# Performance work log

Hardware: AMD Instinct MI355X
Metric: run time of the kernel (lower is better)

## Reference

```python
import jax, jax.numpy as jnp
import numpy as np

N = 100000
E = 1600000
E_OUT = 400000
IN_DIM = 16
HID = 64
OUT_DIM = 2
L = 6
BN_EPS = 1e-5


def setup_inputs() -> dict:
    key = jax.random.key(0)
    ks = jax.random.split(key, 12)
    x = jax.random.normal(ks[0], (N, IN_DIM), dtype=jnp.float32)
    edge_index = jax.random.randint(ks[1], (2, E), 0, N, dtype=jnp.int64)
    edge_index_out = jax.random.randint(ks[2], (2, E_OUT), 0, N, dtype=jnp.int64)
    s_emb = 1.0 / np.sqrt(IN_DIM)
    s_hid = 1.0 / np.sqrt(HID)
    W_emb = jax.random.uniform(ks[3], (IN_DIM, HID), jnp.float32, -s_emb, s_emb)
    b_emb = jax.random.uniform(ks[4], (HID,), jnp.float32, -s_emb, s_emb)
    conv_W = jax.random.uniform(ks[5], (L, HID, HID), jnp.float32, -s_hid, s_hid)
    conv_b = jnp.zeros((L, HID), jnp.float32)
    bn_gamma = jnp.ones((L, HID), jnp.float32)
    bn_beta = jnp.zeros((L, HID), jnp.float32)
    s_fc = 1.0 / np.sqrt(2 * HID)
    fc_W = jax.random.uniform(ks[6], (2 * HID, OUT_DIM), jnp.float32, -s_fc, s_fc)
    fc_b = jax.random.uniform(ks[7], (OUT_DIM,), jnp.float32, -s_fc, s_fc)
    return dict(x=x, edge_index=edge_index, edge_index_out=edge_index_out,
                W_emb=W_emb, b_emb=b_emb, conv_W=conv_W, conv_b=conv_b,
                bn_gamma=bn_gamma, bn_beta=bn_beta, fc_W=fc_W, fc_b=fc_b)


def gcn_conv(h, W, b, src, dst, norm):
    # PyG GCNConv: h' = scatter_add(norm * (hW)[src] -> dst) + b
    hw = h @ W                                   # [N, HID]
    msgs = hw[src] * norm[:, None]               # [E+N, HID] gather
    agg = jax.ops.segment_sum(msgs, dst, num_segments=N)
    return agg + b


def batchnorm_train(h, gamma, beta):
    mean = jnp.mean(h, axis=0)
    var = jnp.mean(jnp.square(h - mean), axis=0)  # biased var (BN training)
    return (h - mean) * jax.lax.rsqrt(var + BN_EPS) * gamma + beta


def reference(x, edge_index, edge_index_out, W_emb, b_emb, conv_W, conv_b,
              bn_gamma, bn_beta, fc_W, fc_b):
    # add self-loops + symmetric normalization (computed once, shared by layers)
    loop = jnp.arange(N, dtype=edge_index.dtype)
    src = jnp.concatenate([edge_index[0], loop])
    dst = jnp.concatenate([edge_index[1], loop])
    deg = jax.ops.segment_sum(jnp.ones_like(dst, dtype=jnp.float32), dst, num_segments=N)
    dinv = jnp.where(deg > 0, jax.lax.rsqrt(jnp.maximum(deg, 1.0)), 0.0)
    norm = dinv[src] * dinv[dst]

    x_embed = x @ W_emb + b_emb                  # node embedding [N, HID]
    for i in range(L):
        h = gcn_conv(x_embed, conv_W[i], conv_b[i], src, dst, norm)
        h = jax.nn.relu(batchnorm_train(h, bn_gamma[i], bn_beta[i]))
        x_embed = x_embed + h                    # residual

    e_src, e_dst = edge_index_out[0], edge_index_out[1]
    edge_repr = jnp.concatenate([x_embed[e_src], x_embed[e_dst]], axis=-1)  # [E_out, 2*HID]
    return edge_repr @ fc_W + fc_b
```

## Files before the change

### kernel.cpp

```cpp
#include <hip/hip_runtime.h>

#define NN 100000
#define NE 1600000
#define NEO 400000
#define HID 64
#define NL 6
#define BN_EPS 1e-5f

#define SPMM_BLOCKS 6250
#define SCAN_BS 512
#define SCAN_NB 196
#define GRP_ROWS 12500
#define BUILD_BPG 784

#define OFF_ECOL 0
#define OFF_XE   NE
#define OFF_AGG  (OFF_XE + NN * 32)
#define OFF_HWB  (OFF_AGG + NN * 32)

#define OD_DINV   0
#define OD_ROWPTR 100352
#define OD_CC     200704
#define OD_BSUM   300704
#define OD_SS     300960
#define OD_SUMS   301088

typedef __attribute__((ext_vector_type(8))) short bf16x8;
typedef __attribute__((ext_vector_type(4))) float f32x4;

static __device__ __forceinline__ unsigned short f2bf(float f) {
    unsigned u = __float_as_uint(f);
    unsigned r = (u + 0x7FFF + ((u >> 16) & 1)) >> 16;
    return (unsigned short)r;
}
static __device__ __forceinline__ float bflo(unsigned u) {
    return __uint_as_float(u << 16);
}
static __device__ __forceinline__ float bfhi(unsigned u) {
    return __uint_as_float(u & 0xFFFF0000u);
}

__global__ void k_hist(const int* __restrict__ dst, int* __restrict__ cnt) {
    int e = blockIdx.x * blockDim.x + threadIdx.x;
    if (e < NE) atomicAdd(&cnt[dst[e]], 1);
}

__global__ void k_scanA(const int* __restrict__ cnt, int* __restrict__ rowptr,
                        int* __restrict__ bsum, float* __restrict__ dinv) {
    __shared__ int sh[SCAN_BS];
    int t = threadIdx.x;
    int i = blockIdx.x * SCAN_BS + t;
    int v = (i < NN) ? cnt[i] : 0;
    sh[t] = v;
    __syncthreads();
    for (int off = 1; off < SCAN_BS; off <<= 1) {
        int a = (t >= off) ? sh[t - off] : 0;
        __syncthreads();
        sh[t] += a;
        __syncthreads();
    }
    if (i < NN) {
        rowptr[i] = sh[t] - v;
        dinv[i] = rsqrtf((float)(v + 1));
    }
    if (t == SCAN_BS - 1) bsum[blockIdx.x] = sh[t];
}

__global__ void k_scanB(int* __restrict__ bsum) {
    __shared__ int sh[256];
    int t = threadIdx.x;
    int v = (t < SCAN_NB) ? bsum[t] : 0;
    sh[t] = v;
    __syncthreads();
    for (int off = 1; off < 256; off <<= 1) {
        int a = (t >= off) ? sh[t - off] : 0;
        __syncthreads();
        sh[t] += a;
        __syncthreads();
    }
    if (t < SCAN_NB) bsum[t] = (t == 0) ? 0 : sh[t - 1];
}

__global__ void k_scanC(int* __restrict__ rowptr, const int* __restrict__ bsum,
                        int* __restrict__ cursor) {
    int i = blockIdx.x * SCAN_BS + threadIdx.x;
    if (i < NN) {
        int rp = rowptr[i] + bsum[blockIdx.x];
        rowptr[i] = rp;
        cursor[i] = rp;
    }
    if (i == 0) rowptr[NN] = NE;
}

__global__ void k_build(const int* __restrict__ src, const int* __restrict__ dst,
                        int* __restrict__ cursor, int* __restrict__ ecol) {
    int g = blockIdx.x & 7;
    int b = blockIdx.x >> 3;
    int lo = g * GRP_ROWS, hi = lo + GRP_ROWS;
    for (int e = b * blockDim.x + threadIdx.x; e < NE; e += BUILD_BPG * blockDim.x) {
        int d = dst[e];
        if (d >= lo && d < hi) {
            int pos = atomicAdd(&cursor[d], 1);
            ecol[pos] = src[e];
        }
    }
}

__global__ void k_embed(const float* __restrict__ x, const float* __restrict__ W,
                        const float* __restrict__ b, unsigned short* __restrict__ xe16) {
    __shared__ float Ws[16 * 64];
    __shared__ float bs[64];
    int t = threadIdx.x;
    for (int i = t; i < 16 * 64; i += 256) Ws[i] = W[i];
    if (t < 64) bs[t] = b[t];
    __syncthreads();
    int c = t & 63, r = t >> 6;
    int n0 = blockIdx.x * 64;
    for (int n = n0 + r; n < n0 + 64 && n < NN; n += 4) {
        const float* xr = x + n * 16;
        float acc = bs[c];
#pragma unroll
        for (int k = 0; k < 16; k++) acc = fmaf(xr[k], Ws[k * 64 + c], acc);
        xe16[(size_t)n * 64 + c] = f2bf(acc);
    }
}

__global__ void k_hw(unsigned short* __restrict__ xe16,
                     const float* __restrict__ W, const float* __restrict__ dinv,
                     const unsigned short* __restrict__ agg16,
                     const float* __restrict__ gamma, const float* __restrict__ beta,
                     const double* __restrict__ sumsPrev, double* __restrict__ sumsCur,
                     unsigned short* __restrict__ hwb, int apply) {
    __shared__ unsigned short Wt[64 * 72];
    __shared__ unsigned short Xb[64 * 72];
    __shared__ float sss[128];
    int t = threadIdx.x;
    int n0 = blockIdx.x * 64;
    if (blockIdx.x == 0) {
        for (int i = t; i < 2048; i += 256) sumsCur[i] = 0.0;
    }
    if (apply && t < 64) {
        double s = 0.0, q = 0.0;
#pragma unroll
        for (int k = 0; k < 16; k++) {
            s += sumsPrev[k * 128 + t];
            q += sumsPrev[k * 128 + 64 + t];
        }
        double mean = s / (double)NN;
        double var = q / (double)NN - mean * mean;
        float sc = gamma[t] * rsqrtf((float)var + BN_EPS);
        sss[t] = sc;
        sss[64 + t] = beta[t] - (float)mean * sc;
    }

    {
        int c = t & 63, r = t >> 6;
#pragma unroll
        for (int jj = 0; jj < 4; jj++) {
            float w0 = W[(r * 16 + jj * 4 + 0) * 64 + c];
            float w1 = W[(r * 16 + jj * 4 + 1) * 64 + c];
            float w2 = W[(r * 16 + jj * 4 + 2) * 64 + c];
            float w3 = W[(r * 16 + jj * 4 + 3) * 64 + c];
            uint2 pk;
            pk.x = ((unsigned)f2bf(w1) << 16) | f2bf(w0);
            pk.y = ((unsigned)f2bf(w3) << 16) | f2bf(w2);
            *(uint2*)&Wt[c * 72 + r * 16 + jj * 4] = pk;
        }
    }
    __syncthreads();

    {
        int n = t >> 2, kq = t & 3;
        int node = n0 + n;
        unsigned xs[8] = {0, 0, 0, 0, 0, 0, 0, 0};
        if (node < NN) {
            const uint4* xr = (const uint4*)(xe16 + (size_t)node * 64 + kq * 16);
            uint4 x0 = xr[0], x1 = xr[1];
            xs[0] = x0.x; xs[1] = x0.y; xs[2] = x0.z; xs[3] = x0.w;
            xs[4] = x1.x; xs[5] = x1.y; xs[6] = x1.z; xs[7] = x1.w;
            if (apply) {
                const uint4* ar = (const uint4*)(agg16 + (size_t)node * 64 + kq * 16);
                uint4 a0 = ar[0], a1 = ar[1];
                unsigned as[8] = {a0.x, a0.y, a0.z, a0.w, a1.x, a1.y, a1.z, a1.w};
                int c = kq * 16;
#pragma unroll
                for (int i = 0; i < 8; i++) {
                    float v0 = bflo(xs[i]) +
                               fmaxf(fmaf(bflo(as[i]), sss[c + 2 * i], sss[64 + c + 2 * i]), 0.f);
                    float v1 = bfhi(xs[i]) +
                               fmaxf(fmaf(bfhi(as[i]), sss[c + 2 * i + 1], sss[64 + c + 2 * i + 1]), 0.f);
                    xs[i] = ((unsigned)f2bf(v1) << 16) | f2bf(v0);
                }
                uint4* xw = (uint4*)(xe16 + (size_t)node * 64 + kq * 16);
                xw[0] = make_uint4(xs[0], xs[1], xs[2], xs[3]);
                xw[1] = make_uint4(xs[4], xs[5], xs[6], xs[7]);
            }
        }
        *(uint4*)&Xb[n * 72 + kq * 16] = make_uint4(xs[0], xs[1], xs[2], xs[3]);
        *(uint4*)&Xb[n * 72 + kq * 16 + 8] = make_uint4(xs[4], xs[5], xs[6], xs[7]);
    }
    __syncthreads();

    int lane = t & 63, w = t >> 6;
    int m = lane & 15, quad = lane >> 4;
    f32x4 acc[4];
#pragma unroll
    for (int tc = 0; tc < 4; tc++) acc[tc] = (f32x4){0.f, 0.f, 0.f, 0.f};
#pragma unroll
    for (int s = 0; s < 2; s++) {
        bf16x8 bfr = *(const bf16x8*)&Xb[(w * 16 + m) * 72 + s * 32 + quad * 8];
#pragma unroll
        for (int tc = 0; tc < 4; tc++) {
            bf16x8 afr = *(const bf16x8*)&Wt[(tc * 16 + m) * 72 + s * 32 + quad * 8];
            acc[tc] = __builtin_amdgcn_mfma_f32_16x16x32_bf16(afr, bfr, acc[tc], 0, 0, 0);
        }
    }
    int node = n0 + w * 16 + m;
    if (node < NN) {
        float di = dinv[node];
#pragma unroll
        for (int tc = 0; tc < 4; tc++) {
            int c0 = tc * 16 + quad * 4;
            uint2 pk;
            pk.x = ((unsigned)f2bf(acc[tc][1] * di) << 16) | f2bf(acc[tc][0] * di);
            pk.y = ((unsigned)f2bf(acc[tc][3] * di) << 16) | f2bf(acc[tc][2] * di);
            *(uint2*)(hwb + (size_t)node * 64 + c0) = pk;
        }
    }
}

__global__ void k_spmm(const int* __restrict__ rowptr, const int* __restrict__ ecol,
                       const unsigned short* __restrict__ hwb, const float* __restrict__ dinv,
                       unsigned short* __restrict__ agg16, double* __restrict__ sums) {
    int t = threadIdx.x;
    int w = t >> 6, l = t & 63;
    int r = l >> 4;
    int sub = (l >> 3) & 1;
    int q = l & 7;
    const uint4* hw4 = (const uint4*)hwb;
    float ls[8], lq[8];
#pragma unroll
    for (int j = 0; j < 8; j++) { ls[j] = 0.f; lq[j] = 0.f; }
    for (int row0 = blockIdx.x * 16 + w * 4; row0 < NN; row0 += SPMM_BLOCKS * 16) {
        int row = row0 + r;
        bool valid = row < NN;
        int p0 = 0, p1 = 0;
        float a[8];
#pragma unroll
        for (int j = 0; j < 8; j++) a[j] = 0.f;
        if (valid) {
            p0 = rowptr[row];
            p1 = rowptr[row + 1];
            if (sub == 0) {
                uint4 sv = hw4[(size_t)row * 8 + q];
                a[0] = bflo(sv.x); a[1] = bfhi(sv.x); a[2] = bflo(sv.y); a[3] = bfhi(sv.y);
                a[4] = bflo(sv.z); a[5] = bfhi(sv.z); a[6] = bflo(sv.w); a[7] = bfhi(sv.w);
            }
        }
        int p = p0 + sub;
        for (; p + 2 < p1; p += 4) {
            int s0 = ecol[p], s1 = ecol[p + 2];
            uint4 u0 = hw4[(size_t)s0 * 8 + q];
            uint4 u1 = hw4[(size_t)s1 * 8 + q];
            a[0] += bflo(u0.x); a[1] += bfhi(u0.x); a[2] += bflo(u0.y); a[3] += bfhi(u0.y);
            a[4] += bflo(u0.z); a[5] += bfhi(u0.z); a[6] += bflo(u0.w); a[7] += bfhi(u0.w);
            a[0] += bflo(u1.x); a[1] += bfhi(u1.x); a[2] += bflo(u1.y); a[3] += bfhi(u1.y);
            a[4] += bflo(u1.z); a[5] += bfhi(u1.z); a[6] += bflo(u1.w); a[7] += bfhi(u1.w);
        }
        if (p < p1) {
            int s0 = ecol[p];
            uint4 u0 = hw4[(size_t)s0 * 8 + q];
            a[0] += bflo(u0.x); a[1] += bfhi(u0.x); a[2] += bflo(u0.y); a[3] += bfhi(u0.y);
            a[4] += bflo(u0.z); a[5] += bfhi(u0.z); a[6] += bflo(u0.w); a[7] += bfhi(u0.w);
        }
#pragma unroll
        for (int j = 0; j < 8; j++) a[j] += __shfl_xor(a[j], 8, 64);
        if (valid && sub == 0) {
            float di = dinv[row];
            unsigned pk[4];
#pragma unroll
            for (int j = 0; j < 4; j++) {
                float v0 = a[2 * j] * di, v1 = a[2 * j + 1] * di;
                pk[j] = ((unsigned)f2bf(v1) << 16) | f2bf(v0);
            }
            *(uint4*)(agg16 + (size_t)row * 64 + 8 * q) = make_uint4(pk[0], pk[1], pk[2], pk[3]);
#pragma unroll
            for (int j = 0; j < 4; j++) {
                float v0 = bflo(pk[j]), v1 = bfhi(pk[j]);
                ls[2 * j] += v0; ls[2 * j + 1] += v1;
                lq[2 * j] = fmaf(v0, v0, lq[2 * j]);
                lq[2 * j + 1] = fmaf(v1, v1, lq[2 * j + 1]);
            }
        }
    }
#pragma unroll
    for (int j = 0; j < 8; j++) {
        ls[j] += __shfl_xor(ls[j], 16, 64); ls[j] += __shfl_xor(ls[j], 32, 64);
        lq[j] += __shfl_xor(lq[j], 16, 64); lq[j] += __shfl_xor(lq[j], 32, 64);
    }
    __shared__ float Ss[4][64], Sq[4][64];
    if (l < 8) {
#pragma unroll
        for (int j = 0; j < 8; j++) {
            Ss[w][8 * l + j] = ls[j];
            Sq[w][8 * l + j] = lq[j];
        }
    }
    __syncthreads();
    if (t < 64) {
        float a = Ss[0][t] + Ss[1][t] + Ss[2][t] + Ss[3][t];
        float b = Sq[0][t] + Sq[1][t] + Sq[2][t] + Sq[3][t];
        double* sh = sums + (blockIdx.x & 15) * 128;
        atomicAdd(&sh[t], (double)a);
        atomicAdd(&sh[64 + t], (double)b);
    }
}

__global__ void k_finalize(const double* __restrict__ sums, const float* __restrict__ gamma,
                           const float* __restrict__ beta, float* __restrict__ ss) {
    int c = threadIdx.x;
    double s = 0.0, q = 0.0;
#pragma unroll
    for (int k = 0; k < 16; k++) { s += sums[k * 128 + c]; q += sums[k * 128 + 64 + c]; }
    double mean = s / (double)NN;
    double var = q / (double)NN - mean * mean;
    float sc = gamma[c] * rsqrtf((float)var + BN_EPS);
    ss[c] = sc;
    ss[64 + c] = beta[c] - (float)mean * sc;
}

__global__ void k_apply(const unsigned short* __restrict__ agg16, const float* __restrict__ ss,
                        unsigned short* __restrict__ xe16) {
    int i = blockIdx.x * blockDim.x + threadIdx.x;
    if (i < NN * 8) {
        int c0 = (i & 7) * 8;
        uint4 av = *(const uint4*)(agg16 + (size_t)i * 8);
        uint4 xv = *(const uint4*)(xe16 + (size_t)i * 8);
        unsigned as[4] = {av.x, av.y, av.z, av.w};
        unsigned xs[4] = {xv.x, xv.y, xv.z, xv.w};
#pragma unroll
        for (int j = 0; j < 4; j++) {
            int c = c0 + 2 * j;
            float v0 = bflo(xs[j]) + fmaxf(fmaf(bflo(as[j]), ss[c], ss[64 + c]), 0.f);
            float v1 = bfhi(xs[j]) + fmaxf(fmaf(bfhi(as[j]), ss[c + 1], ss[64 + c + 1]), 0.f);
            xs[j] = ((unsigned)f2bf(v1) << 16) | f2bf(v0);
        }
        *(uint4*)(xe16 + (size_t)i * 8) = make_uint4(xs[0], xs[1], xs[2], xs[3]);
    }
}

__global__ void k_out(const int* __restrict__ esrc, const int* __restrict__ edst,
                      const unsigned short* __restrict__ xe16, const float* __restrict__ fcW,
                      const float* __restrict__ fcb, float* __restrict__ out) {
    __shared__ float Ws[256];
    __shared__ float bs[2];
    int t = threadIdx.x;
    for (int i = t; i < 256; i += 256) Ws[i] = fcW[i];
    if (t < 2) bs[t] = fcb[t];
    __syncthreads();
    int e = blockIdx.x * blockDim.x + t;
    if (e < NEO) {
        int s = esrc[e], d = edst[e];
        const uint4* rs = (const uint4*)(xe16 + (size_t)s * 64);
        const uint4* rd = (const uint4*)(xe16 + (size_t)d * 64);
        float a0 = bs[0], a1 = bs[1];
#pragma unroll
        for (int i = 0; i < 8; i++) {
            uint4 v = rs[i];
            int c = i * 8;
            a0 += bflo(v.x) * Ws[(c + 0) * 2] + bfhi(v.x) * Ws[(c + 1) * 2] +
                  bflo(v.y) * Ws[(c + 2) * 2] + bfhi(v.y) * Ws[(c + 3) * 2] +
                  bflo(v.z) * Ws[(c + 4) * 2] + bfhi(v.z) * Ws[(c + 5) * 2] +
                  bflo(v.w) * Ws[(c + 6) * 2] + bfhi(v.w) * Ws[(c + 7) * 2];
            a1 += bflo(v.x) * Ws[(c + 0) * 2 + 1] + bfhi(v.x) * Ws[(c + 1) * 2 + 1] +
                  bflo(v.y) * Ws[(c + 2) * 2 + 1] + bfhi(v.y) * Ws[(c + 3) * 2 + 1] +
                  bflo(v.z) * Ws[(c + 4) * 2 + 1] + bfhi(v.z) * Ws[(c + 5) * 2 + 1] +
                  bflo(v.w) * Ws[(c + 6) * 2 + 1] + bfhi(v.w) * Ws[(c + 7) * 2 + 1];
        }
#pragma unroll
        for (int i = 0; i < 8; i++) {
            uint4 v = rd[i];
            int c = 64 + i * 8;
            a0 += bflo(v.x) * Ws[(c + 0) * 2] + bfhi(v.x) * Ws[(c + 1) * 2] +
                  bflo(v.y) * Ws[(c + 2) * 2] + bfhi(v.y) * Ws[(c + 3) * 2] +
                  bflo(v.z) * Ws[(c + 4) * 2] + bfhi(v.z) * Ws[(c + 5) * 2] +
                  bflo(v.w) * Ws[(c + 6) * 2] + bfhi(v.w) * Ws[(c + 7) * 2];
            a1 += bflo(v.x) * Ws[(c + 0) * 2 + 1] + bfhi(v.x) * Ws[(c + 1) * 2 + 1] +
                  bflo(v.y) * Ws[(c + 2) * 2 + 1] + bfhi(v.y) * Ws[(c + 3) * 2 + 1] +
                  bflo(v.z) * Ws[(c + 4) * 2 + 1] + bfhi(v.z) * Ws[(c + 5) * 2 + 1] +
                  bflo(v.w) * Ws[(c + 6) * 2 + 1] + bfhi(v.w) * Ws[(c + 7) * 2 + 1];
        }
        out[e * 2] = a0;
        out[e * 2 + 1] = a1;
    }
}

extern "C" void kernel_launch(void* const* d_in, const int* in_sizes, int n_in,
                              void* d_out, int out_size, void* d_ws, size_t ws_size,
                              hipStream_t stream) {
    const float* x      = (const float*)d_in[0];
    const int*   ei     = (const int*)d_in[1];
    const int*   eio    = (const int*)d_in[2];
    const float* W_emb  = (const float*)d_in[3];
    const float* b_emb  = (const float*)d_in[4];
    const float* conv_W = (const float*)d_in[5];
    const float* bn_g   = (const float*)d_in[7];
    const float* bn_b   = (const float*)d_in[8];
    const float* fc_W   = (const float*)d_in[9];
    const float* fc_b   = (const float*)d_in[10];
    float* out = (float*)d_out;

    float* ws   = (float*)d_ws;
    int*   ecol = (int*)(ws + OFF_ECOL);
    unsigned short* xe16  = (unsigned short*)(ws + OFF_XE);
    unsigned short* agg16 = (unsigned short*)(ws + OFF_AGG);
    unsigned short* hwb   = (unsigned short*)(ws + OFF_HWB);

    float* od     = (float*)d_out;
    float* dinv   = od + OD_DINV;
    int*   rowptr = (int*)(od + OD_ROWPTR);
    int*   cc     = (int*)(od + OD_CC);
    int*   bsum   = (int*)(od + OD_BSUM);
    float* ss     = od + OD_SS;
    double* sums  = (double*)(od + OD_SUMS);

    const int* src  = ei;
    const int* dst  = ei + NE;
    const int* esrc = eio;
    const int* edst = eio + NEO;

    (void)hipMemsetAsync(cc, 0, NN * sizeof(int), stream);
    k_hist<<<(NE + 255) / 256, 256, 0, stream>>>(dst, cc);
    k_scanA<<<SCAN_NB, SCAN_BS, 0, stream>>>(cc, rowptr, bsum, dinv);
    k_scanB<<<1, 256, 0, stream>>>(bsum);
    k_scanC<<<SCAN_NB, SCAN_BS, 0, stream>>>(rowptr, bsum, cc);
    k_build<<<8 * BUILD_BPG, 256, 0, stream>>>(src, dst, cc, ecol);

    k_embed<<<(NN + 63) / 64, 256, 0, stream>>>(x, W_emb, b_emb, xe16);

    for (int l = 0; l < NL; l++) {
        double* sumsPrev = sums + ((l + 1) & 1) * 2048;
        double* sumsCur  = sums + (l & 1) * 2048;
        k_hw<<<(NN + 63) / 64, 256, 0, stream>>>(xe16, conv_W + l * 64 * 64, dinv, agg16,
                                                 bn_g + (l ? (l - 1) * 64 : 0),
                                                 bn_b + (l ? (l - 1) * 64 : 0),
                                                 sumsPrev, sumsCur, hwb, l > 0 ? 1 : 0);
        k_spmm<<<SPMM_BLOCKS, 256, 0, stream>>>(rowptr, ecol, hwb, dinv, agg16, sumsCur);
    }
    k_finalize<<<1, 64, 0, stream>>>(sums + ((NL - 1) & 1) * 2048,
                                     bn_g + (NL - 1) * 64, bn_b + (NL - 1) * 64, ss);
    k_apply<<<(NN * 8 + 255) / 256, 256, 0, stream>>>(agg16, ss, xe16);

    k_out<<<(NEO + 255) / 256, 256, 0, stream>>>(esrc, edst, xe16, fc_W, fc_b, out);
}
```

Baseline: 576.5 us.

## Pre-bin edges by destination group before CSR build

```diff
diff --git a/kernel.cpp b/kernel.cpp
--- a/kernel.cpp
+++ b/kernel.cpp
@@ -11,7 +11,11 @@
 #define SCAN_BS 512
 #define SCAN_NB 196
 #define GRP_ROWS 12500
-#define BUILD_BPG 784
+
+#define BIN_CHUNK 2048
+#define BIN_BLOCKS ((NE + BIN_CHUNK - 1) / BIN_CHUNK)
+#define BIN_CAP 210000
+#define B2_BPG 98
 
 #define OFF_ECOL 0
 #define OFF_XE   NE
@@ -24,6 +28,7 @@
 #define OD_BSUM   300704
 #define OD_SS     300960
 #define OD_SUMS   301088
+#define OD_GCUR   309280
 
 typedef __attribute__((ext_vector_type(8))) short bf16x8;
 typedef __attribute__((ext_vector_type(4))) float f32x4;
@@ -40,9 +45,37 @@
     return __uint_as_float(u & 0xFFFF0000u);
 }
 
-__global__ void k_hist(const int* __restrict__ dst, int* __restrict__ cnt) {
-    int e = blockIdx.x * blockDim.x + threadIdx.x;
-    if (e < NE) atomicAdd(&cnt[dst[e]], 1);
+__global__ void k_bin(const int* __restrict__ src, const int* __restrict__ dst,
+                      int* __restrict__ cnt, int* __restrict__ gcur,
+                      int* __restrict__ bsrc, int* __restrict__ bdst) {
+    __shared__ int cnt8[8], base8[8], off8[8];
+    int t = threadIdx.x;
+    if (t < 8) { cnt8[t] = 0; off8[t] = 0; }
+    __syncthreads();
+    int cb = blockIdx.x * BIN_CHUNK;
+    int s[8], d[8], g[8];
+#pragma unroll
+    for (int j = 0; j < 8; j++) {
+        int e = cb + t + j * 256;
+        s[j] = (e < NE) ? src[e] : -1;
+        d[j] = (e < NE) ? dst[e] : -1;
+        if (d[j] >= 0) {
+            g[j] = (unsigned)d[j] / GRP_ROWS;
+            atomicAdd(&cnt8[g[j]], 1);
+            atomicAdd(&cnt[d[j]], 1);
+        }
+    }
+    __syncthreads();
+    if (t < 8) base8[t] = t * BIN_CAP + atomicAdd(&gcur[t], cnt8[t]);
+    __syncthreads();
+#pragma unroll
+    for (int j = 0; j < 8; j++) {
+        if (d[j] >= 0) {
+            int pos = base8[g[j]] + atomicAdd(&off8[g[j]], 1);
+            bsrc[pos] = s[j];
+            bdst[pos] = d[j];
+        }
+    }
 }
 
 __global__ void k_scanA(const int* __restrict__ cnt, int* __restrict__ rowptr,
@@ -92,17 +125,18 @@
     if (i == 0) rowptr[NN] = NE;
 }
 
-__global__ void k_build(const int* __restrict__ src, const int* __restrict__ dst,
-                        int* __restrict__ cursor, int* __restrict__ ecol) {
+__global__ void k_build2(const int* __restrict__ gcur, const int* __restrict__ bsrc,
+                         const int* __restrict__ bdst, int* __restrict__ cursor,
+                         int* __restrict__ ecol) {
     int g = blockIdx.x & 7;
     int b = blockIdx.x >> 3;
-    int lo = g * GRP_ROWS, hi = lo + GRP_ROWS;
-    for (int e = b * blockDim.x + threadIdx.x; e < NE; e += BUILD_BPG * blockDim.x) {
-        int d = dst[e];
-        if (d >= lo && d < hi) {
-            int pos = atomicAdd(&cursor[d], 1);
-            ecol[pos] = src[e];
-        }
+    int n = gcur[g];
+    int base = g * BIN_CAP;
+    for (int i = b * blockDim.x + threadIdx.x; i < n; i += B2_BPG * blockDim.x) {
+        int d = bdst[base + i];
+        int s = bsrc[base + i];
+        int pos = atomicAdd(&cursor[d], 1);
+        ecol[pos] = s;
     }
 }
 
@@ -415,6 +449,8 @@
     unsigned short* xe16  = (unsigned short*)(ws + OFF_XE);
     unsigned short* agg16 = (unsigned short*)(ws + OFF_AGG);
     unsigned short* hwb   = (unsigned short*)(ws + OFF_HWB);
+    int* bsrc = (int*)(ws + OFF_XE);
+    int* bdst = (int*)(ws + OFF_AGG);
 
     float* od     = (float*)d_out;
     float* dinv   = od + OD_DINV;
@@ -423,6 +459,7 @@
     int*   bsum   = (int*)(od + OD_BSUM);
     float* ss     = od + OD_SS;
     double* sums  = (double*)(od + OD_SUMS);
+    int*   gcur   = (int*)(od + OD_GCUR);
 
     const int* src  = ei;
     const int* dst  = ei + NE;
@@ -430,11 +467,12 @@
     const int* edst = eio + NEO;
 
     (void)hipMemsetAsync(cc, 0, NN * sizeof(int), stream);
-    k_hist<<<(NE + 255) / 256, 256, 0, stream>>>(dst, cc);
+    (void)hipMemsetAsync(gcur, 0, 8 * sizeof(int), stream);
+    k_bin<<<BIN_BLOCKS, 256, 0, stream>>>(src, dst, cc, gcur, bsrc, bdst);
     k_scanA<<<SCAN_NB, SCAN_BS, 0, stream>>>(cc, rowptr, bsum, dinv);
     k_scanB<<<1, 256, 0, stream>>>(bsum);
     k_scanC<<<SCAN_NB, SCAN_BS, 0, stream>>>(rowptr, bsum, cc);
-    k_build<<<8 * BUILD_BPG, 256, 0, stream>>>(src, dst, cc, ecol);
+    k_build2<<<8 * B2_BPG, 256, 0, stream>>>(gcur, bsrc, bdst, cc, ecol);
 
     k_embed<<<(NN + 63) / 64, 256, 0, stream>>>(x, W_emb, b_emb, xe16);
 
```

Result: no change. 584.9 us (+1.5%).
